# Performance work log

Measured on AMD Instinct MI355X. Metric: run time of the kernel, lower is better.

The kernel has to match this reference:

```python
import jax, jax.numpy as jnp
import numpy as np

B, S, H = 64, 512, 1024  # batch, seq_len, hidden (input_size == hidden_size per source)


def setup_inputs() -> dict:
    key = jax.random.key(0)
    k1, k2 = jax.random.split(key)
    x = jax.random.normal(k1, (B, S, H), dtype=jnp.float32)
    # xavier_uniform_ for U: bound = sqrt(6/(fan_in+fan_out))
    bound = float(np.sqrt(6.0 / (H + 4 * H)))
    U = jax.random.uniform(k2, (H, 4 * H), dtype=jnp.float32, minval=-bound, maxval=bound)
    bias = jnp.zeros((4 * H,), dtype=jnp.float32)
    return {"x": x, "U": U, "bias": bias}


def reference(x, U, bias):
    # Faithful LSTM recurrence (peephole=False; note: W is declared in the
    # original module but never used in forward, and the gate matmul uses U
    # on the input x_t, exactly as in the source).
    batch = x.shape[0]
    HS = U.shape[0]
    h0 = jnp.zeros((batch, HS), dtype=x.dtype)
    c0 = jnp.zeros((batch, HS), dtype=x.dtype)

    def step(carry, x_t):
        h_t, c_t = carry
        gates = x_t @ U + bias  # [B, 4H]
        i_t = jax.nn.sigmoid(gates[:, :HS])
        f_t = jax.nn.sigmoid(gates[:, HS:2 * HS])
        g_t = jnp.tanh(gates[:, 2 * HS:3 * HS])
        o_t = jax.nn.sigmoid(gates[:, 3 * HS:])
        c_t = f_t * c_t + i_t * g_t
        h_t = o_t * jnp.tanh(c_t)
        return (h_t, c_t), h_t

    (h_T, c_T), hs = jax.lax.scan(step, (h0, c0), jnp.swapaxes(x, 0, 1))  # hs: [S, B, H]
    hidden_sequence = jnp.swapaxes(hs, 0, 1)  # [B, S, H]
    return hidden_sequence, (h_T, c_T)
```

## Files before the change

kernel.cpp:

```cpp
#include <hip/hip_runtime.h>
#include <hip/hip_bf16.h>
#include <stdint.h>

typedef __bf16 bf16x8 __attribute__((ext_vector_type(8)));
typedef float  f32x4  __attribute__((ext_vector_type(4)));
typedef unsigned short u16x8 __attribute__((ext_vector_type(8)));

#define HS    1024
#define FOURH 4096
#define SEQ   512
#define BATCH 64

#define BAR()  asm volatile("s_barrier" ::: "memory")
#define VMW(n) asm volatile("s_waitcnt vmcnt(" #n ")" ::: "memory")

__device__ __forceinline__ unsigned short f2bf(float f) {
    unsigned u = __builtin_bit_cast(unsigned, f);
    u = (u + 0x7FFFu + ((u >> 16) & 1u)) >> 16;
    return (unsigned short)u;
}

__device__ __forceinline__ void gload_lds16(const void* g, void* l) {
    __builtin_amdgcn_global_load_lds(
        (const __attribute__((address_space(1))) void*)g,
        (__attribute__((address_space(3))) void*)l, 16, 0, 0);
}

__global__ __launch_bounds__(256) void convert_x(const float* __restrict__ x,
                                                 unsigned short* __restrict__ xb,
                                                 long n8) {
    long i = (long)blockIdx.x * blockDim.x + threadIdx.x;
    long stride = (long)gridDim.x * blockDim.x;
    for (; i < n8; i += stride) {
        const float4* p = (const float4*)(x + i * 8);
        float4 a = p[0], b = p[1];
        u16x8 o;
        o[0] = f2bf(a.x); o[1] = f2bf(a.y); o[2] = f2bf(a.z); o[3] = f2bf(a.w);
        o[4] = f2bf(b.x); o[5] = f2bf(b.y); o[6] = f2bf(b.z); o[7] = f2bf(b.w);
        *(u16x8*)(xb + i * 8) = o;
    }
}

__global__ __launch_bounds__(256) void transpose_u(const float* __restrict__ U,
                                                   unsigned short* __restrict__ Ut) {
    __shared__ float tile[32][33];
    int bx = blockIdx.x;
    int tn = bx >> 5;
    int tk = bx & 31;
    int c = threadIdx.x & 31;
    int r = threadIdx.x >> 5;
#pragma unroll
    for (int i = 0; i < 4; ++i) {
        int k = tk * 32 + r + i * 8;
        tile[r + i * 8][c] = U[(size_t)k * FOURH + tn * 32 + c];
    }
    __syncthreads();
#pragma unroll
    for (int i = 0; i < 4; ++i) {
        int nl = r + i * 8;
        Ut[(size_t)(tn * 32 + nl) * HS + tk * 32 + c] = f2bf(tile[c][nl]);
    }
}

__global__ __launch_bounds__(512, 1) void gemm_gates8(
    const unsigned short* __restrict__ Xb,
    const unsigned short* __restrict__ Ut,
    const float* __restrict__ bias,
    _Float16* __restrict__ gates,
    int lg2chunk, int s0) {
    __shared__ unsigned short LDSU[65536];

    int nwg = gridDim.x;
    int bid = blockIdx.x;
    int wg = (bid & 7) * (nwg >> 3) + (bid >> 3);
    int mt = wg >> 4;
    int nt = wg & 15;

    int tid = threadIdx.x;
    int w = tid >> 6, l = tid & 63;
    int wr = w >> 2, wc = w & 3;
    int lr = l & 15, lg = l >> 4;

    const int m0 = mt * 256, n0 = nt * 256;
    const int cmask = (1 << lg2chunk) - 1;

    const int rdo = lr * 32 + ((lg * 8) ^ ((lr & 8) << 1));

    const int srow = l >> 2;
    const int skin = ((l & 3) * 8) ^ (((l >> 5) & 1) << 4);

    const unsigned short* pAq[4];
    const unsigned short* pBq[4];
#pragma unroll
    for (int q = 0; q < 4; ++q) {
        int rowg = q * 64 + (w >> 1) * 16 + srow;
        int mrow = m0 + rowg;
        int b = mrow >> lg2chunk, sl2 = mrow & cmask;
        pAq[q] = Xb + (size_t)(b * SEQ + s0 + sl2) * HS + (w & 1) * 32 + skin;
        pBq[q] = Ut + (size_t)(n0 + rowg) * HS + (w & 1) * 32 + skin;
    }
    const int dsub = (w >> 1) * 2 + (w & 1);

    f32x4 acc[8][4];
#pragma unroll
    for (int mi = 0; mi < 8; ++mi)
#pragma unroll
        for (int ni = 0; ni < 4; ++ni) acc[mi][ni] = 0.f;

#define SA(T, Q) gload_lds16(pAq[Q] + (T) * 64, \
        &LDSU[(((T) & 1) << 15) + ((Q) * 8 + dsub) * 512])
#define SB(T, Q) gload_lds16(pBq[Q] + (T) * 64, \
        &LDSU[(((T) & 1) << 15) + 16384 + ((Q) * 8 + dsub) * 512])

    bf16x8 aq[2][4], bn0[2][2], bn1[2][2];

#define RDA(MH) \
    _Pragma("unroll") for (int ks = 0; ks < 2; ++ks) \
    _Pragma("unroll") for (int mi = 0; mi < 4; ++mi) \
        aq[ks][mi] = *(const bf16x8*)(buf + ((wr * 8 + (MH) * 4 + mi) * 2 + ks) * 512 + rdo)
#define RDB(NH, BN) \
    _Pragma("unroll") for (int ks = 0; ks < 2; ++ks) \
    _Pragma("unroll") for (int ni = 0; ni < 2; ++ni) \
        BN[ks][ni] = *(const bf16x8*)(buf + 16384 + ((wc * 4 + (NH) * 2 + ni) * 2 + ks) * 512 + rdo)
#define MMQ(MH, NH, BN) \
    __builtin_amdgcn_s_setprio(1); \
    _Pragma("unroll") for (int ks = 0; ks < 2; ++ks) \
    _Pragma("unroll") for (int mi = 0; mi < 4; ++mi) \
    _Pragma("unroll") for (int ni = 0; ni < 2; ++ni) \
        acc[(MH) * 4 + mi][(NH) * 2 + ni] = __builtin_amdgcn_mfma_f32_16x16x32_bf16( \
            aq[ks][mi], BN[ks][ni], acc[(MH) * 4 + mi][(NH) * 2 + ni], 0, 0, 0); \
    __builtin_amdgcn_s_setprio(0)

    SA(0, 0); SA(0, 2); SB(0, 0); SB(0, 1); SB(0, 2); SB(0, 3); SA(0, 1); SA(0, 3);
    VMW(2); BAR();

    for (int t = 0; t < 16; ++t) {
        const unsigned short* buf = &LDSU[(t & 1) << 15];
        RDA(0);
        RDB(0, bn0);
        if (t < 15) { SA(t + 1, 0); SA(t + 1, 2); }
        MMQ(0, 0, bn0);
        RDB(1, bn1);
        if (t < 15) { SB(t + 1, 0); SB(t + 1, 1); }
        MMQ(0, 1, bn1);
        if (t < 15) { VMW(4); } else { VMW(0); }
        BAR();
        RDA(1);
        if (t < 15) { SB(t + 1, 2); SB(t + 1, 3); }
        MMQ(1, 1, bn1);
        if (t < 15) { SA(t + 1, 1); SA(t + 1, 3); }
        MMQ(1, 0, bn0);
        if (t < 15) { VMW(2); }
        BAR();
    }

    _Float16* T = (_Float16*)LDSU;
#pragma unroll
    for (int ni = 0; ni < 4; ++ni) {
        int col = wc * 64 + ni * 16 + lr;
        int gcol = n0 + col;
        bool is_g = ((gcol >> 10) == 2);
        float bv = bias[gcol];
#pragma unroll
        for (int mi = 0; mi < 8; ++mi) {
#pragma unroll
            for (int r = 0; r < 4; ++r) {
                int row = wr * 128 + mi * 16 + lg * 4 + r;
                float v = acc[mi][ni][r] + bv;
                float e;
                if (is_g) e = 1.f - 2.f / (1.f + __expf(2.f * v));
                else      e = 1.f / (1.f + __expf(-v));
                T[row * 256 + (col ^ (((row >> 2) & 3) << 4))] = (_Float16)e;
            }
        }
    }
    BAR();
#pragma unroll
    for (int p = 0; p < 16; ++p) {
        int q = p * 512 + tid;
        int row = q >> 5, s = q & 31;
        int cs = (s * 8) ^ (((row >> 2) & 3) << 4);
        uint4 val = *(const uint4*)(T + row * 256 + cs);
        *(uint4*)(gates + (size_t)(m0 + row) * FOURH + n0 + s * 8) = val;
    }
#undef SA
#undef SB
#undef RDA
#undef RDB
#undef MMQ
}

__global__ __launch_bounds__(256) void lstm_recur(
    const _Float16* __restrict__ gates,
    float* __restrict__ out,
    float* __restrict__ cstate,
    int chunk, int s0) {
    int t = blockIdx.x * 256 + threadIdx.x;
    int b = t >> 10, h = t & 1023;
    float c = (s0 == 0) ? 0.f : cstate[t];
    const _Float16* gp = gates + (size_t)b * chunk * FOURH + h;
    float* op = out + (size_t)(b * SEQ + s0) * HS + h;
    float hv = 0.f;
    for (int sl = 0; sl < chunk; sl += 8) {
        float iv[8], fv[8], gv[8], ov[8];
#pragma unroll
        for (int u = 0; u < 8; ++u) {
            const _Float16* q = gp + (size_t)(sl + u) * FOURH;
            iv[u] = (float)q[0];
            fv[u] = (float)q[1024];
            gv[u] = (float)q[2048];
            ov[u] = (float)q[3072];
        }
#pragma unroll
        for (int u = 0; u < 8; ++u) {
            c = fv[u] * c + iv[u] * gv[u];
            float th = 1.f - 2.f / (1.f + __expf(2.f * c));
            hv = ov[u] * th;
            op[(size_t)(sl + u) * HS] = hv;
        }
    }
    cstate[t] = c;
    if (s0 + chunk == SEQ) {
        out[(size_t)BATCH * SEQ * HS + t] = hv;
        out[(size_t)BATCH * SEQ * HS + BATCH * HS + t] = c;
    }
}

extern "C" void kernel_launch(void* const* d_in, const int* in_sizes, int n_in,
                              void* d_out, int out_size, void* d_ws, size_t ws_size,
                              hipStream_t stream) {
    const float* x    = (const float*)d_in[0];
    const float* U    = (const float*)d_in[1];
    const float* bias = (const float*)d_in[2];
    float* out = (float*)d_out;
    char*  ws  = (char*)d_ws;

    unsigned short* Xb = (unsigned short*)ws;
    unsigned short* Ut = (unsigned short*)(ws + 67108864);
    float* cstate      = (float*)(ws + 75497472);
    _Float16* gates    = (_Float16*)(ws + 75759616);
    const size_t fixed = 75759616;

    int chunk = 512;
    while (chunk > 4 && fixed + (size_t)BATCH * chunk * FOURH * 2 > ws_size)
        chunk >>= 1;
    int lg2 = 31 - __builtin_clz(chunk);

    convert_x<<<2048, 256, 0, stream>>>(x, Xb, (long)BATCH * SEQ * HS / 8);
    transpose_u<<<4096, 256, 0, stream>>>(U, Ut);

    for (int s0 = 0; s0 < SEQ; s0 += chunk) {
        int mtiles = (BATCH * chunk) / 256;
        gemm_gates8<<<mtiles * 16, 512, 0, stream>>>(Xb, Ut, bias, gates, lg2, s0);
        lstm_recur<<<256, 256, 0, stream>>>(gates, out, cstate, chunk, s0);
    }
}
```

Before: 454.5 us.

## Store gates in 4-timestep packed layout and use fast reciprocal activations

The GEMM epilogue now writes gate values straight from registers into a layout that groups four consecutive timesteps per column as one 8-byte vector. This drops the LDS transpose staging and its barrier. The recurrence kernel then reads f16x4 vectors instead of scalar halves, so each load carries more useful bytes. Sigmoid and tanh switch to the hardware approximate reciprocal, which adds a small amount of rounding error. The 8-byte global stores from the GEMM are less coalesced than the previous 16-byte row stores.

```diff
diff --git a/kernel.cpp b/kernel.cpp
--- a/kernel.cpp
+++ b/kernel.cpp
@@ -5,6 +5,8 @@
 typedef __bf16 bf16x8 __attribute__((ext_vector_type(8)));
 typedef float  f32x4  __attribute__((ext_vector_type(4)));
 typedef unsigned short u16x8 __attribute__((ext_vector_type(8)));
+typedef unsigned short u16x4 __attribute__((ext_vector_type(4)));
+typedef _Float16 f16x4 __attribute__((ext_vector_type(4)));
 
 #define HS    1024
 #define FOURH 4096
@@ -24,6 +26,13 @@
     __builtin_amdgcn_global_load_lds(
         (const __attribute__((address_space(1))) void*)g,
         (__attribute__((address_space(3))) void*)l, 16, 0, 0);
+}
+
+__device__ __forceinline__ float fsigmoid(float v) {
+    return __builtin_amdgcn_rcpf(1.f + __expf(-v));
+}
+__device__ __forceinline__ float ftanh(float v) {
+    return 1.f - 2.f * __builtin_amdgcn_rcpf(1.f + __expf(2.f * v));
 }
 
 __global__ __launch_bounds__(256) void convert_x(const float* __restrict__ x,
@@ -154,34 +163,23 @@
         BAR();
     }
 
-    _Float16* T = (_Float16*)LDSU;
 #pragma unroll
     for (int ni = 0; ni < 4; ++ni) {
-        int col = wc * 64 + ni * 16 + lr;
-        int gcol = n0 + col;
+        int gcol = n0 + wc * 64 + ni * 16 + lr;
         bool is_g = ((gcol >> 10) == 2);
         float bv = bias[gcol];
 #pragma unroll
         for (int mi = 0; mi < 8; ++mi) {
+            int rg = ((m0 + wr * 128 + mi * 16) >> 2) + lg;
+            u16x4 pk;
 #pragma unroll
             for (int r = 0; r < 4; ++r) {
-                int row = wr * 128 + mi * 16 + lg * 4 + r;
                 float v = acc[mi][ni][r] + bv;
-                float e;
-                if (is_g) e = 1.f - 2.f / (1.f + __expf(2.f * v));
-                else      e = 1.f / (1.f + __expf(-v));
-                T[row * 256 + (col ^ (((row >> 2) & 3) << 4))] = (_Float16)e;
+                float e = is_g ? ftanh(v) : fsigmoid(v);
+                pk[r] = __builtin_bit_cast(unsigned short, (_Float16)e);
             }
+            *(u16x4*)(gates + ((size_t)rg * FOURH + gcol) * 4) = pk;
         }
-    }
-    BAR();
-#pragma unroll
-    for (int p = 0; p < 16; ++p) {
-        int q = p * 512 + tid;
-        int row = q >> 5, s = q & 31;
-        int cs = (s * 8) ^ (((row >> 2) & 3) << 4);
-        uint4 val = *(const uint4*)(T + row * 256 + cs);
-        *(uint4*)(gates + (size_t)(m0 + row) * FOURH + n0 + s * 8) = val;
     }
 #undef SA
 #undef SB
@@ -198,25 +196,29 @@
     int t = blockIdx.x * 256 + threadIdx.x;
     int b = t >> 10, h = t & 1023;
     float c = (s0 == 0) ? 0.f : cstate[t];
-    const _Float16* gp = gates + (size_t)b * chunk * FOURH + h;
+    const _Float16* gp = gates + ((size_t)((b * chunk) >> 2) * FOURH + h) * 4;
     float* op = out + (size_t)(b * SEQ + s0) * HS + h;
     float hv = 0.f;
-    for (int sl = 0; sl < chunk; sl += 8) {
-        float iv[8], fv[8], gv[8], ov[8];
-#pragma unroll
-        for (int u = 0; u < 8; ++u) {
-            const _Float16* q = gp + (size_t)(sl + u) * FOURH;
-            iv[u] = (float)q[0];
-            fv[u] = (float)q[1024];
-            gv[u] = (float)q[2048];
-            ov[u] = (float)q[3072];
+    const int ng = chunk >> 2;
+    for (int g4 = 0; g4 < ng; g4 += 2) {
+        f16x4 iv[2], fv[2], gv[2], ov[2];
+#pragma unroll
+        for (int u = 0; u < 2; ++u) {
+            const _Float16* q = gp + (size_t)(g4 + u) * (FOURH * 4);
+            iv[u] = *(const f16x4*)(q);
+            fv[u] = *(const f16x4*)(q + 4096);
+            gv[u] = *(const f16x4*)(q + 8192);
+            ov[u] = *(const f16x4*)(q + 12288);
         }
 #pragma unroll
-        for (int u = 0; u < 8; ++u) {
-            c = fv[u] * c + iv[u] * gv[u];
-            float th = 1.f - 2.f / (1.f + __expf(2.f * c));
-            hv = ov[u] * th;
-            op[(size_t)(sl + u) * HS] = hv;
+        for (int u = 0; u < 2; ++u) {
+#pragma unroll
+            for (int r = 0; r < 4; ++r) {
+                c = (float)fv[u][r] * c + (float)iv[u][r] * (float)gv[u][r];
+                float th = ftanh(c);
+                hv = (float)ov[u][r] * th;
+                op[(size_t)((g4 + u) * 4 + r) * HS] = hv;
+            }
         }
     }
     cstate[t] = c;
```

New measurement: 399.8 us. -12.0%, faster.
